# Optimization experiments

Measured on AMD Instinct MI355X. Metric: run time of the kernel, lower is better.

Reference implementation:

```python
import jax, jax.numpy as jnp
import numpy as np

DIM = 32
HID = 128          # edge-MLP hidden width
N = 8192           # total nodes
E = 131072         # total edges
B = 64             # number of graphs
NUM_MP = 3
S2S_STEPS = 3


def setup_inputs() -> dict:
    key = jax.random.key(0)
    ks = jax.random.split(key, 24)
    g = lambda k, shape, s=0.05: jax.random.normal(k, shape, dtype=jnp.float32) * s

    inp = {
        "x": jax.random.normal(ks[0], (N, 1), dtype=jnp.float32),
        "edge_attr": jax.random.uniform(ks[1], (E, 2), dtype=jnp.float32),
        # params
        "lin0_w": g(ks[2], (1, DIM)), "lin0_b": g(ks[3], (DIM,)),
        "enn_w1": g(ks[4], (2, HID)), "enn_b1": g(ks[5], (HID,)),
        "enn_w2": g(ks[6], (HID, DIM * DIM)), "enn_b2": g(ks[7], (DIM * DIM,)),
        "root_w": g(ks[8], (DIM, DIM)), "conv_b": g(ks[9], (DIM,)),
        # GRU (gates ordered r,z,n as in torch)
        "gru_wih": g(ks[10], (DIM, 3 * DIM)), "gru_whh": g(ks[11], (DIM, 3 * DIM)),
        "gru_bih": g(ks[12], (3 * DIM,)), "gru_bhh": g(ks[13], (3 * DIM,)),
        # Set2Set LSTM: input 2*DIM, hidden DIM (gates ordered i,f,g,o as in torch)
        "s2s_wih": g(ks[14], (2 * DIM, 4 * DIM)), "s2s_whh": g(ks[15], (DIM, 4 * DIM)),
        "s2s_bih": g(ks[16], (4 * DIM,)), "s2s_bhh": g(ks[17], (4 * DIM,)),
        "lin1_w": g(ks[18], (2 * DIM, DIM)), "lin1_b": g(ks[19], (DIM,)),
        "lin2_w": g(ks[20], (DIM, 1)), "lin2_b": g(ks[21], (1,)),
        # int args
        "edge_index": jax.random.randint(ks[22], (2, E), 0, N, dtype=jnp.int32),
        "batch": jnp.sort(jax.random.randint(ks[23], (N,), 0, B, dtype=jnp.int32)),
    }
    return inp


def _forward(x, edge_attr, lin0_w, lin0_b, enn_w1, enn_b1, enn_w2, enn_b2,
             root_w, conv_b, gru_wih, gru_whh, gru_bih, gru_bhh,
             s2s_wih, s2s_whh, s2s_bih, s2s_bhh, lin1_w, lin1_b, lin2_w, lin2_b,
             edge_index, batch):
    src, dst = edge_index[0], edge_index[1]

    out = jax.nn.relu(x @ lin0_w + lin0_b)          # [N, DIM]
    h = out                                          # GRU hidden state

    # edge-conditioned weights (constant across MP layers -> hoisted)
    ew = jax.nn.relu(edge_attr @ enn_w1 + enn_b1) @ enn_w2 + enn_b2
    W = ew.reshape(E, DIM, DIM)                      # [E, in, out]

    deg = jnp.maximum(jax.ops.segment_sum(jnp.ones((E,), jnp.float32), dst,
                                          num_segments=N), 1.0)[:, None]

    for _ in range(NUM_MP):
        # NNConv: gather -> per-edge small matmul -> scatter-mean, + root + bias
        msg = jnp.einsum('ed,edo->eo', out[src], W)  # [E, DIM]
        agg = jax.ops.segment_sum(msg, dst, num_segments=N) / deg
        m = jax.nn.relu(agg + out @ root_w + conv_b)
        # GRU cell (single step)
        gi = m @ gru_wih + gru_bih
        gh = h @ gru_whh + gru_bhh
        ir, iz, in_ = jnp.split(gi, 3, axis=-1)
        hr, hz, hn = jnp.split(gh, 3, axis=-1)
        r = jax.nn.sigmoid(ir + hr)
        z = jax.nn.sigmoid(iz + hz)
        n = jnp.tanh(in_ + r * hn)
        h = (1.0 - z) * n + z * h
        out = h

    # Set2Set pooling
    qh = jnp.zeros((B, DIM), jnp.float32)
    qc = jnp.zeros((B, DIM), jnp.float32)
    q_star = jnp.zeros((B, 2 * DIM), jnp.float32)
    for _ in range(S2S_STEPS):
        gates = q_star @ s2s_wih + s2s_bih + qh @ s2s_whh + s2s_bhh
        i_, f_, g_, o_ = jnp.split(gates, 4, axis=-1)
        qc = jax.nn.sigmoid(f_) * qc + jax.nn.sigmoid(i_) * jnp.tanh(g_)
        qh = jax.nn.sigmoid(o_) * jnp.tanh(qc)       # [B, DIM]
        e = jnp.sum(out * qh[batch], axis=-1)        # [N] attention logits
        emax = jax.ops.segment_max(e, batch, num_segments=B)
        a = jnp.exp(e - emax[batch])
        a = a / jax.ops.segment_sum(a, batch, num_segments=B)[batch]
        r_read = jax.ops.segment_sum(a[:, None] * out, batch, num_segments=B)
        q_star = jnp.concatenate([qh, r_read], axis=-1)  # [B, 2*DIM]

    y = jax.nn.relu(q_star @ lin1_w + lin1_b) @ lin2_w + lin2_b
    return y.reshape(-1)                              # [B]


def reference(x, edge_attr, lin0_w, lin0_b, enn_w1, enn_b1, enn_w2, enn_b2,
              root_w, conv_b, gru_wih, gru_whh, gru_bih, gru_bhh,
              s2s_wih, s2s_whh, s2s_bih, s2s_bhh, lin1_w, lin1_b, lin2_w, lin2_b,
              edge_index, batch):
    return _forward(x, edge_attr, lin0_w, lin0_b, enn_w1, enn_b1, enn_w2, enn_b2,
                    root_w, conv_b, gru_wih, gru_whh, gru_bih, gru_bhh,
                    s2s_wih, s2s_whh, s2s_bih, s2s_bhh, lin1_w, lin1_b, lin2_w,
                    lin2_b, edge_index, batch)
```

## Files before the change

### kernel.cpp

```cpp
#include <hip/hip_runtime.h>

#define N_NODES 8192
#define N_EDGES 131072
#define NGRAPH  64
#define DIM     32
#define HID     128
#define KFULL   128
#define G_NODES 4
#define SROW    36

__device__ __forceinline__ float sigmoidf_(float x) { return 1.0f / (1.0f + expf(-x)); }

__global__ void prep1_kernel(const float* __restrict__ x, const float* __restrict__ w,
                             const float* __restrict__ b, float* __restrict__ out,
                             const int* __restrict__ dst, int* __restrict__ counts) {
  const int bb = blockIdx.x;
  if (bb < 1024) {
    int idx = bb * 256 + threadIdx.x;
    int n = idx >> 5, d = idx & 31;
    out[idx] = fmaxf(fmaf(x[n], w[d], b[d]), 0.0f);
  } else {
    int e = (bb - 1024) * 256 + threadIdx.x;
    atomicAdd(&counts[dst[e]], 1);
  }
}

__global__ void scan_kernel(const int* __restrict__ counts,
                            int* __restrict__ offsets,
                            float* __restrict__ deg_inv) {
  __shared__ int sm[1024];
  int t = threadIdx.x;
  int base = t * 8;
  int loc[8];
  int s = 0;
#pragma unroll
  for (int i = 0; i < 8; ++i) { loc[i] = s; s += counts[base + i]; }
  sm[t] = s;
  __syncthreads();
  for (int off = 1; off < 1024; off <<= 1) {
    int v = (t >= off) ? sm[t - off] : 0;
    __syncthreads();
    sm[t] += v;
    __syncthreads();
  }
  int excl = (t > 0) ? sm[t - 1] : 0;
#pragma unroll
  for (int i = 0; i < 8; ++i) {
    offsets[base + i] = excl + loc[i];
    int c = counts[base + i];
    deg_inv[base + i] = 1.0f / (float)(c > 0 ? c : 1);
  }
  if (t == 1023) offsets[N_NODES] = sm[1023];
}

__global__ void prep2_kernel(const int* __restrict__ ei, const float* __restrict__ ea,
                             const int* __restrict__ offsets, int* __restrict__ cursor,
                             int* __restrict__ csr_src, float2* __restrict__ csr_ea,
                             const int* __restrict__ batch, int* __restrict__ gstart) {
  const int bb = blockIdx.x;
  if (bb < 512) {
    int e = bb * 256 + threadIdx.x;
    int d = ei[N_EDGES + e];
    int pos = atomicAdd(&cursor[d], 1);
    int slot = offsets[d] + pos;
    csr_src[slot] = ei[e];
    csr_ea[slot] = make_float2(ea[2 * e], ea[2 * e + 1]);
  } else {
    int n = (bb - 512) * 256 + threadIdx.x;
    int b = batch[n];
    if (n == 0) {
      for (int g = 0; g <= b; ++g) gstart[g] = 0;
    } else {
      int bp = batch[n - 1];
      for (int g = bp + 1; g <= b; ++g) gstart[g] = n;
    }
    if (n == N_NODES - 1) {
      for (int g = b + 1; g <= NGRAPH; ++g) gstart[g] = N_NODES;
    }
  }
}

__global__ __launch_bounds__(256, 2) void mp_full_kernel(
    const float* __restrict__ out_cur, const int* __restrict__ offsets,
    const int* __restrict__ csr_src, const float2* __restrict__ csr_ea,
    const float* __restrict__ w1, const float* __restrict__ b1,
    const float* __restrict__ w2, const float* __restrict__ b2,
    const float* __restrict__ deg_inv, const float* __restrict__ root_w,
    const float* __restrict__ conv_b, const float* __restrict__ gwih,
    const float* __restrict__ gwhh, const float* __restrict__ gbih,
    const float* __restrict__ gbhh, float* __restrict__ out_nxt) {
  constexpr int C = 32;
  __shared__ float smem[G_NODES * KFULL * SROW];
  float* S = smem;
  float* hidb = smem;
  float* osrcb = smem + C * KFULL;
  float* red = smem;
  float* ob  = smem + 4352;
  float* hb  = smem + 4480;
  float* mb  = smem + 4608;
  float* b2s = smem + 4736;
  __shared__ int offs[G_NODES + 1];

  const int t = threadIdx.x;
  const int node0 = blockIdx.x * G_NODES;

  if (t <= G_NODES) offs[t] = offsets[node0 + t];

  const int kg = t >> 3, dg = t & 7;
  const int k0 = kg * 4, d0 = dg * 4;
  const int ec = t >> 3, sub = t & 7;

  float w1x[16], w1y[16], b1v[16];
#pragma unroll
  for (int i = 0; i < 16; ++i) {
    const int kgl = sub * 16 + i;
    w1x[i] = w1[kgl];
    w1y[i] = w1[HID + kgl];
    b1v[i] = b1[kgl];
  }

  float acc[G_NODES][4][4];
#pragma unroll
  for (int g = 0; g < G_NODES; ++g)
#pragma unroll
    for (int i = 0; i < 4; ++i)
#pragma unroll
      for (int j = 0; j < 4; ++j) acc[g][i][j] = 0.0f;
  float oacc[G_NODES] = {};
  __syncthreads();

#pragma unroll
  for (int g = 0; g < G_NODES; ++g) {
    const int base = offs[g], end = offs[g + 1];
    for (int c0 = base; c0 < end; c0 += C) {
      const int cnt = min(C, end - c0);
      __syncthreads();
      if (ec < cnt) {
        const int slot = c0 + ec;
        const float2 eav = csr_ea[slot];
        const int sidx = csr_src[slot];
        float hv[16];
#pragma unroll
        for (int i = 0; i < 16; ++i)
          hv[i] = fmaxf(fmaf(eav.y, w1y[i], fmaf(eav.x, w1x[i], b1v[i])), 0.0f);
#pragma unroll
        for (int j = 0; j < 4; ++j)
          *(float4*)(hidb + ec * KFULL + sub * 16 + j * 4) =
              make_float4(hv[j * 4], hv[j * 4 + 1], hv[j * 4 + 2], hv[j * 4 + 3]);
        *(float4*)(osrcb + ec * DIM + sub * 4) =
            *(const float4*)(out_cur + sidx * DIM + sub * 4);
      }
      __syncthreads();
      for (int e = 0; e < cnt; ++e) {
        const float4 hvv = *(const float4*)(hidb + e * KFULL + k0);
        const float4 ov = *(const float4*)(osrcb + e * DIM + d0);
        acc[g][0][0] = fmaf(hvv.x, ov.x, acc[g][0][0]);
        acc[g][0][1] = fmaf(hvv.x, ov.y, acc[g][0][1]);
        acc[g][0][2] = fmaf(hvv.x, ov.z, acc[g][0][2]);
        acc[g][0][3] = fmaf(hvv.x, ov.w, acc[g][0][3]);
        acc[g][1][0] = fmaf(hvv.y, ov.x, acc[g][1][0]);
        acc[g][1][1] = fmaf(hvv.y, ov.y, acc[g][1][1]);
        acc[g][1][2] = fmaf(hvv.y, ov.z, acc[g][1][2]);
        acc[g][1][3] = fmaf(hvv.y, ov.w, acc[g][1][3]);
        acc[g][2][0] = fmaf(hvv.z, ov.x, acc[g][2][0]);
        acc[g][2][1] = fmaf(hvv.z, ov.y, acc[g][2][1]);
        acc[g][2][2] = fmaf(hvv.z, ov.z, acc[g][2][2]);
        acc[g][2][3] = fmaf(hvv.z, ov.w, acc[g][2][3]);
        acc[g][3][0] = fmaf(hvv.w, ov.x, acc[g][3][0]);
        acc[g][3][1] = fmaf(hvv.w, ov.y, acc[g][3][1]);
        acc[g][3][2] = fmaf(hvv.w, ov.z, acc[g][3][2]);
        acc[g][3][3] = fmaf(hvv.w, ov.w, acc[g][3][3]);
        if (t < DIM) oacc[g] += osrcb[e * DIM + t];
      }
    }
  }
  __syncthreads();

  {
    const int shift = (kg & 3) * 8;
    const int dd = (d0 + shift) & 31;
#pragma unroll
    for (int g = 0; g < G_NODES; ++g) {
      float* Sg = S + g * KFULL * SROW;
#pragma unroll
      for (int i = 0; i < 4; ++i)
        *(float4*)(Sg + (k0 + i) * SROW + dd) =
            make_float4(acc[g][i][0], acc[g][i][1], acc[g][i][2], acc[g][i][3]);
    }
  }
  __syncthreads();

  {
    const int ks = t >> 4;
    const int dvh = (t >> 3) & 1;
    const int og = t & 7;
    float a4[G_NODES][4];
#pragma unroll
    for (int g = 0; g < G_NODES; ++g)
#pragma unroll
      for (int r = 0; r < 4; ++r) a4[g][r] = 0.0f;
#pragma unroll
    for (int i = 0; i < 8; ++i) {
      const int kl = ks * 8 + i;
      const int shift = ((kl >> 2) & 3) * 8;
      const float* w2k = w2 + (size_t)kl * (DIM * DIM);
#pragma unroll
      for (int q = 0; q < 4; ++q) {
        const int dbase = dvh * 16 + q * 4;
        const int dq = (dbase + shift) & 31;
        const int soff = kl * SROW + dq;
        const float4 sv0 = *(const float4*)(S + 0 * KFULL * SROW + soff);
        const float4 sv1 = *(const float4*)(S + 1 * KFULL * SROW + soff);
        const float4 sv2 = *(const float4*)(S + 2 * KFULL * SROW + soff);
        const float4 sv3 = *(const float4*)(S + 3 * KFULL * SROW + soff);
        const float* s0 = (const float*)&sv0;
        const float* s1 = (const float*)&sv1;
        const float* s2 = (const float*)&sv2;
        const float* s3 = (const float*)&sv3;
#pragma unroll
        for (int r = 0; r < 4; ++r) {
          const float4 wv = *(const float4*)(w2k + (dbase + r) * DIM + og * 4);
          a4[0][0] = fmaf(s0[r], wv.x, a4[0][0]);
          a4[0][1] = fmaf(s0[r], wv.y, a4[0][1]);
          a4[0][2] = fmaf(s0[r], wv.z, a4[0][2]);
          a4[0][3] = fmaf(s0[r], wv.w, a4[0][3]);
          a4[1][0] = fmaf(s1[r], wv.x, a4[1][0]);
          a4[1][1] = fmaf(s1[r], wv.y, a4[1][1]);
          a4[1][2] = fmaf(s1[r], wv.z, a4[1][2]);
          a4[1][3] = fmaf(s1[r], wv.w, a4[1][3]);
          a4[2][0] = fmaf(s2[r], wv.x, a4[2][0]);
          a4[2][1] = fmaf(s2[r], wv.y, a4[2][1]);
          a4[2][2] = fmaf(s2[r], wv.z, a4[2][2]);
          a4[2][3] = fmaf(s2[r], wv.w, a4[2][3]);
          a4[3][0] = fmaf(s3[r], wv.x, a4[3][0]);
          a4[3][1] = fmaf(s3[r], wv.y, a4[3][1]);
          a4[3][2] = fmaf(s3[r], wv.z, a4[3][2]);
          a4[3][3] = fmaf(s3[r], wv.w, a4[3][3]);
        }
      }
    }
    __syncthreads();
#pragma unroll
    for (int g = 0; g < G_NODES; ++g)
#pragma unroll
      for (int r = 0; r < 4; ++r) red[(g * 4 + r) * 257 + t] = a4[g][r];
  }
  if (t < DIM) {
#pragma unroll
    for (int g = 0; g < G_NODES; ++g) ob[g * DIM + t] = oacc[g];
  }
  if (t < G_NODES * DIM) hb[t] = out_cur[node0 * DIM + t];
#pragma unroll
  for (int i = 0; i < 4; ++i) b2s[i * 256 + t] = b2[i * 256 + t];
  __syncthreads();

  if (t < G_NODES * DIM) {
    const int g = t >> 5, o = t & 31;
    const int og2 = o >> 2, r2 = o & 3;
    const float* rp = red + (g * 4 + r2) * 257 + og2;
    float agg = 0.0f;
#pragma unroll
    for (int j = 0; j < 32; ++j) agg += rp[j * 8];
#pragma unroll
    for (int d = 0; d < DIM; ++d) agg = fmaf(ob[g * DIM + d], b2s[d * DIM + o], agg);
    agg *= deg_inv[node0 + g];
    float rt = conv_b[o];
#pragma unroll
    for (int d = 0; d < DIM; ++d) rt = fmaf(hb[g * DIM + d], root_w[d * DIM + o], rt);
    mb[t] = fmaxf(agg + rt, 0.0f);
  }
  __syncthreads();
  if (t < G_NODES * DIM) {
    const int g = t >> 5, o = t & 31;
    float gi[3], gh[3];
#pragma unroll
    for (int jj = 0; jj < 3; ++jj) {
      float si = gbih[jj * DIM + o], sh = gbhh[jj * DIM + o];
#pragma unroll
      for (int d = 0; d < DIM; ++d) {
        si = fmaf(mb[g * DIM + d], gwih[d * 3 * DIM + jj * DIM + o], si);
        sh = fmaf(hb[g * DIM + d], gwhh[d * 3 * DIM + jj * DIM + o], sh);
      }
      gi[jj] = si;
      gh[jj] = sh;
    }
    const float r = sigmoidf_(gi[0] + gh[0]);
    const float z = sigmoidf_(gi[1] + gh[1]);
    const float nn = tanhf(fmaf(r, gh[2], gi[2]));
    out_nxt[(node0 * DIM) + t] = (1.0f - z) * nn + z * hb[t];
  }
}

__global__ __launch_bounds__(256) void s2s_kernel(
    const float* __restrict__ outf, const int* __restrict__ gstart,
    const float* __restrict__ wih, const float* __restrict__ whh,
    const float* __restrict__ bih, const float* __restrict__ bhh,
    const float* __restrict__ l1w, const float* __restrict__ l1b,
    const float* __restrict__ l2w, const float* __restrict__ l2b,
    float* __restrict__ y) {
  __shared__ float qh[DIM], qc[DIM], qstar[2 * DIM], gates[4 * DIM];
  __shared__ float wsum[4], wmax[4], wr[4][DIM];
  const int b = blockIdx.x, t = threadIdx.x;
  const int gs = gstart[b], ge = gstart[b + 1];
  const int w = t >> 6, lane = t & 63;
  if (t < DIM) { qh[t] = 0.0f; qc[t] = 0.0f; }
  if (t < 2 * DIM) qstar[t] = 0.0f;
  __syncthreads();
  for (int step = 0; step < 3; ++step) {
    if (t < 4 * DIM) {
      float gv = bih[t] + bhh[t];
      for (int i = 0; i < 2 * DIM; ++i) gv = fmaf(qstar[i], wih[i * 4 * DIM + t], gv);
      for (int i = 0; i < DIM; ++i) gv = fmaf(qh[i], whh[i * 4 * DIM + t], gv);
      gates[t] = gv;
    }
    __syncthreads();
    if (t < DIM) {
      const float ig = sigmoidf_(gates[t]);
      const float fg = sigmoidf_(gates[DIM + t]);
      const float gg = tanhf(gates[2 * DIM + t]);
      const float og = sigmoidf_(gates[3 * DIM + t]);
      const float c = fmaf(fg, qc[t], ig * gg);
      qc[t] = c;
      qh[t] = og * tanhf(c);
    }
    __syncthreads();
    float lmax = -INFINITY;
    for (int n = gs + t; n < ge; n += 256) {
      const float* orow = outf + n * DIM;
      float e = 0.0f;
#pragma unroll
      for (int d = 0; d < DIM; ++d) e = fmaf(orow[d], qh[d], e);
      lmax = fmaxf(lmax, e);
    }
#pragma unroll
    for (int off = 32; off > 0; off >>= 1) lmax = fmaxf(lmax, __shfl_xor(lmax, off));
    if (lane == 0) wmax[w] = lmax;
    __syncthreads();
    const float gmax = fmaxf(fmaxf(wmax[0], wmax[1]), fmaxf(wmax[2], wmax[3]));
    float rl[DIM];
#pragma unroll
    for (int d = 0; d < DIM; ++d) rl[d] = 0.0f;
    float lsum = 0.0f;
    for (int n = gs + t; n < ge; n += 256) {
      const float* orow = outf + n * DIM;
      float e = 0.0f;
#pragma unroll
      for (int d = 0; d < DIM; ++d) e = fmaf(orow[d], qh[d], e);
      const float a = expf(e - gmax);
      lsum += a;
#pragma unroll
      for (int d = 0; d < DIM; ++d) rl[d] = fmaf(a, orow[d], rl[d]);
    }
#pragma unroll
    for (int off = 32; off > 0; off >>= 1) {
      lsum += __shfl_xor(lsum, off);
#pragma unroll
      for (int d = 0; d < DIM; ++d) rl[d] += __shfl_xor(rl[d], off);
    }
    __syncthreads();
    if (lane == 0) {
      wsum[w] = lsum;
#pragma unroll
      for (int d = 0; d < DIM; ++d) wr[w][d] = rl[d];
    }
    __syncthreads();
    if (t < DIM) {
      const float stot = wsum[0] + wsum[1] + wsum[2] + wsum[3];
      const float rv = wr[0][t] + wr[1][t] + wr[2][t] + wr[3][t];
      qstar[t] = qh[t];
      qstar[DIM + t] = (stot > 0.0f) ? rv / stot : 0.0f;
    }
    __syncthreads();
  }
  if (t < DIM) {
    float u = l1b[t];
    for (int i = 0; i < 2 * DIM; ++i) u = fmaf(qstar[i], l1w[i * DIM + t], u);
    u = fmaxf(u, 0.0f);
    float v = u * l2w[t];
#pragma unroll
    for (int off = 16; off > 0; off >>= 1) v += __shfl_xor(v, off);
    if (t == 0) y[b] = v + l2b[0];
  }
}

extern "C" void kernel_launch(void* const* d_in, const int* in_sizes, int n_in,
                              void* d_out, int out_size, void* d_ws, size_t ws_size,
                              hipStream_t stream) {
  const float* x        = (const float*)d_in[0];
  const float* ea       = (const float*)d_in[1];
  const float* lin0_w   = (const float*)d_in[2];
  const float* lin0_b   = (const float*)d_in[3];
  const float* enn_w1   = (const float*)d_in[4];
  const float* enn_b1   = (const float*)d_in[5];
  const float* enn_w2   = (const float*)d_in[6];
  const float* enn_b2   = (const float*)d_in[7];
  const float* root_w   = (const float*)d_in[8];
  const float* conv_b   = (const float*)d_in[9];
  const float* gru_wih  = (const float*)d_in[10];
  const float* gru_whh  = (const float*)d_in[11];
  const float* gru_bih  = (const float*)d_in[12];
  const float* gru_bhh  = (const float*)d_in[13];
  const float* s2s_wih  = (const float*)d_in[14];
  const float* s2s_whh  = (const float*)d_in[15];
  const float* s2s_bih  = (const float*)d_in[16];
  const float* s2s_bhh  = (const float*)d_in[17];
  const float* lin1_w   = (const float*)d_in[18];
  const float* lin1_b   = (const float*)d_in[19];
  const float* lin2_w   = (const float*)d_in[20];
  const float* lin2_b   = (const float*)d_in[21];
  const int*   ei       = (const int*)d_in[22];
  const int*   batch    = (const int*)d_in[23];
  float* y = (float*)d_out;

  char* p = (char*)d_ws;
  auto alloc = [&](size_t bytes) -> void* {
    void* r = (void*)p;
    p += (bytes + 255) & ~(size_t)255;
    return r;
  };
  float*  out_a   = (float*)alloc(N_NODES * DIM * 4);
  float*  out_b   = (float*)alloc(N_NODES * DIM * 4);
  int*    counts  = (int*)alloc(N_NODES * 4);
  int*    offsets = (int*)alloc((N_NODES + 1) * 4);
  int*    cursor  = (int*)alloc(N_NODES * 4);
  int*    csr_src = (int*)alloc(N_EDGES * 4);
  float2* csr_ea  = (float2*)alloc(N_EDGES * 8);
  float*  deg_inv = (float*)alloc(N_NODES * 4);
  int*    gstart  = (int*)alloc((NGRAPH + 1) * 4);
  (void)ws_size; (void)n_in; (void)in_sizes; (void)out_size;

  hipMemsetAsync(counts, 0, N_NODES * 4, stream);
  hipMemsetAsync(cursor, 0, N_NODES * 4, stream);

  prep1_kernel<<<1024 + 512, 256, 0, stream>>>(x, lin0_w, lin0_b, out_a,
                                               ei + N_EDGES, counts);
  scan_kernel<<<1, 1024, 0, stream>>>(counts, offsets, deg_inv);
  prep2_kernel<<<512 + 32, 256, 0, stream>>>(ei, ea, offsets, cursor, csr_src,
                                             csr_ea, batch, gstart);

  const int ngroups = N_NODES / G_NODES;
  const float* cur = out_a;
  float* nxt = out_b;
  for (int layer = 0; layer < 3; ++layer) {
    mp_full_kernel<<<ngroups, 256, 0, stream>>>(
        cur, offsets, csr_src, csr_ea, enn_w1, enn_b1, enn_w2, enn_b2,
        deg_inv, root_w, conv_b, gru_wih, gru_whh, gru_bih, gru_bhh, nxt);
    const float* tmp = cur; cur = nxt; nxt = (float*)tmp;
  }

  s2s_kernel<<<NGRAPH, 256, 0, stream>>>(cur, gstart, s2s_wih, s2s_whh, s2s_bih,
                                         s2s_bhh, lin1_w, lin1_b, lin2_w, lin2_b, y);
}
```

Measured before the change: 444.1 us.

## Stage edge-MLP contraction in two K halves to halve shared memory

```diff
diff --git a/kernel.cpp b/kernel.cpp
--- a/kernel.cpp
+++ b/kernel.cpp
@@ -6,6 +6,7 @@
 #define DIM     32
 #define HID     128
 #define KFULL   128
+#define KHALF   64
 #define G_NODES 4
 #define SROW    36
 
@@ -80,7 +81,7 @@
   }
 }
 
-__global__ __launch_bounds__(256, 2) void mp_full_kernel(
+__global__ __launch_bounds__(256, 4) void mp_layer_kernel(
     const float* __restrict__ out_cur, const int* __restrict__ offsets,
     const int* __restrict__ csr_src, const float2* __restrict__ csr_ea,
     const float* __restrict__ w1, const float* __restrict__ b1,
@@ -90,7 +91,7 @@
     const float* __restrict__ gwhh, const float* __restrict__ gbih,
     const float* __restrict__ gbhh, float* __restrict__ out_nxt) {
   constexpr int C = 32;
-  __shared__ float smem[G_NODES * KFULL * SROW];
+  __shared__ float smem[G_NODES * KHALF * SROW];
   float* S = smem;
   float* hidb = smem;
   float* osrcb = smem + C * KFULL;
@@ -176,43 +177,45 @@
   }
   __syncthreads();
 
-  {
-    const int shift = (kg & 3) * 8;
-    const int dd = (d0 + shift) & 31;
-#pragma unroll
-    for (int g = 0; g < G_NODES; ++g) {
-      float* Sg = S + g * KFULL * SROW;
-#pragma unroll
-      for (int i = 0; i < 4; ++i)
-        *(float4*)(Sg + (k0 + i) * SROW + dd) =
-            make_float4(acc[g][i][0], acc[g][i][1], acc[g][i][2], acc[g][i][3]);
-    }
-  }
-  __syncthreads();
-
-  {
-    const int ks = t >> 4;
-    const int dvh = (t >> 3) & 1;
-    const int og = t & 7;
-    float a4[G_NODES][4];
-#pragma unroll
-    for (int g = 0; g < G_NODES; ++g)
-#pragma unroll
-      for (int r = 0; r < 4; ++r) a4[g][r] = 0.0f;
-#pragma unroll
-    for (int i = 0; i < 8; ++i) {
-      const int kl = ks * 8 + i;
-      const int shift = ((kl >> 2) & 3) * 8;
-      const float* w2k = w2 + (size_t)kl * (DIM * DIM);
+  const int ks = t >> 4;
+  const int dvh = (t >> 3) & 1;
+  const int og = t & 7;
+  float a4[G_NODES][4];
+#pragma unroll
+  for (int g = 0; g < G_NODES; ++g)
+#pragma unroll
+    for (int r = 0; r < 4; ++r) a4[g][r] = 0.0f;
+
+#pragma unroll
+  for (int p = 0; p < 2; ++p) {
+    if ((kg >> 4) == p) {
+      const int kgl4 = (kg & 15) * 4;
+      const int shift = (kg & 3) * 8;
+      const int dd = (d0 + shift) & 31;
+#pragma unroll
+      for (int g = 0; g < G_NODES; ++g) {
+        float* Sg = S + g * KHALF * SROW;
+#pragma unroll
+        for (int i = 0; i < 4; ++i)
+          *(float4*)(Sg + (kgl4 + i) * SROW + dd) =
+              make_float4(acc[g][i][0], acc[g][i][1], acc[g][i][2], acc[g][i][3]);
+      }
+    }
+    __syncthreads();
+#pragma unroll
+    for (int i = 0; i < 4; ++i) {
+      const int kl = ks * 4 + i;
+      const int shift = (ks & 3) * 8;
+      const float* w2k = w2 + (size_t)(p * KHALF + kl) * (DIM * DIM);
 #pragma unroll
       for (int q = 0; q < 4; ++q) {
         const int dbase = dvh * 16 + q * 4;
         const int dq = (dbase + shift) & 31;
         const int soff = kl * SROW + dq;
-        const float4 sv0 = *(const float4*)(S + 0 * KFULL * SROW + soff);
-        const float4 sv1 = *(const float4*)(S + 1 * KFULL * SROW + soff);
-        const float4 sv2 = *(const float4*)(S + 2 * KFULL * SROW + soff);
-        const float4 sv3 = *(const float4*)(S + 3 * KFULL * SROW + soff);
+        const float4 sv0 = *(const float4*)(S + 0 * KHALF * SROW + soff);
+        const float4 sv1 = *(const float4*)(S + 1 * KHALF * SROW + soff);
+        const float4 sv2 = *(const float4*)(S + 2 * KHALF * SROW + soff);
+        const float4 sv3 = *(const float4*)(S + 3 * KHALF * SROW + soff);
         const float* s0 = (const float*)&sv0;
         const float* s1 = (const float*)&sv1;
         const float* s2 = (const float*)&sv2;
@@ -240,11 +243,12 @@
       }
     }
     __syncthreads();
-#pragma unroll
-    for (int g = 0; g < G_NODES; ++g)
-#pragma unroll
-      for (int r = 0; r < 4; ++r) red[(g * 4 + r) * 257 + t] = a4[g][r];
-  }
+  }
+
+#pragma unroll
+  for (int g = 0; g < G_NODES; ++g)
+#pragma unroll
+    for (int r = 0; r < 4; ++r) red[(g * 4 + r) * 257 + t] = a4[g][r];
   if (t < DIM) {
 #pragma unroll
     for (int g = 0; g < G_NODES; ++g) ob[g * DIM + t] = oacc[g];
@@ -287,7 +291,7 @@
     const float r = sigmoidf_(gi[0] + gh[0]);
     const float z = sigmoidf_(gi[1] + gh[1]);
     const float nn = tanhf(fmaf(r, gh[2], gi[2]));
-    out_nxt[(node0 * DIM) + t] = (1.0f - z) * nn + z * hb[t];
+    out_nxt[node0 * DIM + t] = (1.0f - z) * nn + z * hb[t];
   }
 }
 
@@ -421,16 +425,15 @@
   float*  out_a   = (float*)alloc(N_NODES * DIM * 4);
   float*  out_b   = (float*)alloc(N_NODES * DIM * 4);
   int*    counts  = (int*)alloc(N_NODES * 4);
+  int*    cursor  = (int*)alloc(N_NODES * 4);
   int*    offsets = (int*)alloc((N_NODES + 1) * 4);
-  int*    cursor  = (int*)alloc(N_NODES * 4);
   int*    csr_src = (int*)alloc(N_EDGES * 4);
   float2* csr_ea  = (float2*)alloc(N_EDGES * 8);
   float*  deg_inv = (float*)alloc(N_NODES * 4);
   int*    gstart  = (int*)alloc((NGRAPH + 1) * 4);
   (void)ws_size; (void)n_in; (void)in_sizes; (void)out_size;
 
-  hipMemsetAsync(counts, 0, N_NODES * 4, stream);
-  hipMemsetAsync(cursor, 0, N_NODES * 4, stream);
+  hipMemsetAsync(counts, 0, 2 * N_NODES * 4, stream);
 
   prep1_kernel<<<1024 + 512, 256, 0, stream>>>(x, lin0_w, lin0_b, out_a,
                                                ei + N_EDGES, counts);
@@ -442,7 +445,7 @@
   const float* cur = out_a;
   float* nxt = out_b;
   for (int layer = 0; layer < 3; ++layer) {
-    mp_full_kernel<<<ngroups, 256, 0, stream>>>(
+    mp_layer_kernel<<<ngroups, 256, 0, stream>>>(
         cur, offsets, csr_src, csr_ea, enn_w1, enn_b1, enn_w2, enn_b2,
         deg_inv, root_w, conv_b, gru_wih, gru_whh, gru_bih, gru_bhh, nxt);
     const float* tmp = cur; cur = nxt; nxt = (float*)tmp;
```

Result: slower. 557.1 us (+25.4%).
